# Optimization experiments

Measured on AMD Instinct MI355X. Metric: run time of the kernel, lower is better.

## Reference

```python
import jax, jax.numpy as jnp
import numpy as np

B, T, E, H, R = 1, 2048, 4096, 16, 64
D = E // H
SCALE_ATTN = float(np.sqrt(D))


def _i8_linear(x, W, b, alpha, beta):
    # W8A8B8O8Linear: int8 in, int8 weight/bias, int8 out with requant epilogue
    acc = jnp.einsum('bte,oe->bto', x.astype(jnp.int32), W.astype(jnp.int32)).astype(jnp.float32)
    y = alpha * acc + beta * b.astype(jnp.float32)
    return jnp.clip(jnp.round(y), -128, 127).astype(jnp.int8)


def _rotate_every_two(x):
    x1, x2 = x[..., ::2], x[..., 1::2]
    return jnp.stack([-x2, x1], axis=-1).reshape(x.shape)


def _sincos(seq_len, dim):
    inv_freq = 1.0 / (10000.0 ** (jnp.arange(0, dim, 2, dtype=jnp.float32) / dim))
    ang = jnp.arange(seq_len, dtype=jnp.float32)[:, None] * inv_freq[None, :]
    return jnp.sin(ang), jnp.cos(ang)


def _apply_rotary(x, sin, cos):
    # duplicate_interleave -> repeat each freq twice along last dim
    sin = jnp.repeat(sin, 2, axis=-1)[None, :, None, :]
    cos = jnp.repeat(cos, 2, axis=-1)[None, :, None, :]
    return x * cos + _rotate_every_two(x) * sin


def setup_inputs():
    key = jax.random.key(0)
    ks = jax.random.split(key, 9)
    i8 = lambda k, s: jax.random.randint(k, s, -128, 128, dtype=jnp.int32).astype(jnp.int8)
    return {
        'hidden_states': i8(ks[0], (B, T, E)),
        'Wq': i8(ks[1], (E, E)), 'bq': i8(ks[2], (E,)),
        'Wk': i8(ks[3], (E, E)), 'bk': i8(ks[4], (E,)),
        'Wv': i8(ks[5], (E, E)), 'bv': i8(ks[6], (E,)),
        'Wo': i8(ks[7], (E, E)),
        'b_out': jax.random.normal(ks[8], (E,), dtype=jnp.float32),
        'alpha_q': 2e-4, 'beta_q': 1.0,
        'alpha_k': 2e-4, 'beta_k': 1.0,
        'alpha_v': 2e-4, 'beta_v': 1.0,
        'alpha_qk': 1e-3, 'alpha_pv': 1e-2, 'alpha_out': 2e-4,
    }


def reference(hidden_states, Wq, bq, Wk, bk, Wv, bv, Wo, b_out,
              alpha_q, beta_q, alpha_k, beta_k, alpha_v, beta_v,
              alpha_qk, alpha_pv, alpha_out):
    # int8 q/k/v projections -> [B, T, H, D]
    q = _i8_linear(hidden_states, Wq, bq, alpha_q, beta_q).reshape(B, T, H, D)
    k = _i8_linear(hidden_states, Wk, bk, alpha_k, beta_k).reshape(B, T, H, D)
    v = _i8_linear(hidden_states, Wv, bv, alpha_v, beta_v).reshape(B, T, H, D)
    v = v.transpose(0, 2, 1, 3)  # [B, H, T, D] int8

    # fused rotary on first R dims (float math on dequantized-per-tensor int8 codes)
    sin, cos = _sincos(T, R)
    qf, kf = q.astype(jnp.float32), k.astype(jnp.float32)
    qf = jnp.concatenate([_apply_rotary(qf[..., :R], sin, cos), qf[..., R:]], axis=-1)
    kf = jnp.concatenate([_apply_rotary(kf[..., :R], sin, cos), kf[..., R:]], axis=-1)
    # torch .to(int8) truncates toward zero
    to_i8 = lambda x: jnp.clip(jnp.trunc(x), -128, 127).astype(jnp.int8)
    q = to_i8(qf.transpose(0, 2, 1, 3))  # [B, H, T, D]
    k = to_i8(kf.transpose(0, 2, 1, 3))

    scores = alpha_qk * jnp.einsum('bhtd,bhsd->bhts', q.astype(jnp.int32), k.astype(jnp.int32)).astype(jnp.float32)
    causal = jnp.tril(jnp.ones((T, T), dtype=bool))
    scores = jnp.where(causal, scores, jnp.finfo(jnp.float32).min)
    probs = jax.nn.softmax(scores / SCALE_ATTN, axis=-1)
    probs = jnp.round(probs * 127.0).astype(jnp.int8)  # requant probs to int8

    acc = jnp.einsum('bhts,bhsd->bhtd', probs.astype(jnp.int32), v.astype(jnp.int32)).astype(jnp.float32)
    attn_out = jnp.clip(jnp.round(alpha_pv * acc), -128, 127).astype(jnp.int8)
    attn_out = attn_out.transpose(0, 2, 1, 3).reshape(B, T, E)  # merge heads

    # W8A8BFP32OFP32Linear
    out = alpha_out * jnp.einsum('bte,oe->bto', attn_out.astype(jnp.int32), Wo.astype(jnp.int32)).astype(jnp.float32) + b_out
    return out
```

## Files before the change

kernel.cpp:

```cpp
#include <hip/hip_runtime.h>
#include <cstdint>
#include <cmath>

#define T_ 2048
#define E_ 4096
#define H_ 16
#define D_ 256
#define NF 32

typedef int v4i  __attribute__((ext_vector_type(4)));

__device__ __forceinline__ int dot4(int a, int b, int c) {
#if __has_builtin(__builtin_amdgcn_sdot4)
  return __builtin_amdgcn_sdot4(a, b, c, false);
#else
  c += ((a << 24) >> 24) * ((b << 24) >> 24);
  c += ((a << 16) >> 24) * ((b << 16) >> 24);
  c += ((a <<  8) >> 24) * ((b <<  8) >> 24);
  c += (a >> 24) * (b >> 24);
  return c;
#endif
}

__device__ __forceinline__ int pack4i(int4 v) {
  return (v.x & 255) | ((v.y & 255) << 8) | ((v.z & 255) << 16) | (v.w << 24);
}

#define GLD_LDS16(g, l)                                                        \
  __builtin_amdgcn_global_load_lds(                                            \
      (const __attribute__((address_space(1))) void*)(g),                      \
      (__attribute__((address_space(3))) void*)(l), 16, 0, 0)

__global__ void sincos_kernel(float* __restrict__ sinT, float* __restrict__ cosT) {
  int idx = blockIdx.x * 256 + threadIdx.x;
  int t = idx >> 5, j = idx & 31;
  float invf = (float)exp(-(double)j * (log(10000.0) / 32.0));
  float ang = (float)t * invf;
  sinT[idx] = (float)sin((double)ang);
  cosT[idx] = (float)cos((double)ang);
}

__global__ __launch_bounds__(256) void repack_kernel(const int* __restrict__ src,
                                                     int8_t* __restrict__ dst) {
  size_t i = (size_t)blockIdx.x * 256 + threadIdx.x;
  const int4* s = (const int4*)src + i * 4;
  int4 a = s[0], b = s[1], c = s[2], d = s[3];
  int4 o;
  o.x = pack4i(a); o.y = pack4i(b); o.z = pack4i(c); o.w = pack4i(d);
  ((int4*)dst)[i] = o;
}

__global__ __launch_bounds__(256, 3) void qkv_gemm_mfma(
    const int8_t* __restrict__ x8,
    const int8_t* __restrict__ Wq8, const int* __restrict__ bq,
    const int8_t* __restrict__ Wk8, const int* __restrict__ bk,
    const int8_t* __restrict__ Wv8, const int* __restrict__ bv,
    const float* __restrict__ alpq, const float* __restrict__ betq,
    const float* __restrict__ alpk, const float* __restrict__ betk,
    const float* __restrict__ alpv, const float* __restrict__ betv,
    int8_t* __restrict__ Q8, int8_t* __restrict__ K8, int8_t* __restrict__ VT)
{
  const int mode = blockIdx.z;
  const int8_t* __restrict__ W = (mode == 0) ? Wq8 : (mode == 1 ? Wk8 : Wv8);
  const int* __restrict__ bs   = (mode == 0) ? bq  : (mode == 1 ? bk  : bv);
  const float alpha = (mode == 0) ? alpq[0] : (mode == 1 ? alpk[0] : alpv[0]);
  const float beta  = (mode == 0) ? betq[0] : (mode == 1 ? betk[0] : betv[0]);

  __shared__ int8_t As[3][8192];
  __shared__ int8_t Bs[3][8192];

  const int tid  = threadIdx.x;
  const int wave = tid >> 6, lane = tid & 63;
  const int wm = wave >> 1, wn = wave & 1;
  const int t0 = blockIdx.x * 128, o0 = blockIdx.y * 128;

  const int srow = lane >> 2;
  const int scol = ((lane & 3) ^ ((lane >> 3) & 3)) * 16;
  const int col  = lane & 15;
  const int quad = lane >> 4;

  v4i acc[4][4] = {};

  const int8_t* gA0 = x8 + (size_t)(t0 + wave * 32 + srow) * E_ + scol;
  const int8_t* gB0 = W  + (size_t)(o0 + wave * 32 + srow) * E_ + scol;

#define STAGE_QKV(bufi, kt) do {                                               \
    const int e0_ = (kt) * 64;                                                 \
    GLD_LDS16(gA0 + e0_,           As[bufi] + wave * 2048);                    \
    GLD_LDS16(gA0 + e0_ + 16 * E_, As[bufi] + wave * 2048 + 1024);             \
    GLD_LDS16(gB0 + e0_,           Bs[bufi] + wave * 2048);                    \
    GLD_LDS16(gB0 + e0_ + 16 * E_, Bs[bufi] + wave * 2048 + 1024);             \
  } while (0)

  int aoff[4], boff[4];
  #pragma unroll
  for (int i = 0; i < 4; ++i) {
    const int ra = wm * 64 + i * 16 + col;
    aoff[i] = ra * 64 + ((quad ^ ((ra >> 1) & 3)) * 16);
    const int rb = wn * 64 + i * 16 + col;
    boff[i] = rb * 64 + ((quad ^ ((rb >> 1) & 3)) * 16);
  }

  STAGE_QKV(0, 0);
  STAGE_QKV(1, 1);

  int cur = 0;
  for (int kt = 0; kt < 64; ++kt) {
    if (kt == 63) asm volatile("s_waitcnt vmcnt(0)" ::: "memory");
    else          asm volatile("s_waitcnt vmcnt(4)" ::: "memory");
    __builtin_amdgcn_s_barrier();
    if (kt < 62) {
      int nb = cur + 2; if (nb >= 3) nb -= 3;
      STAGE_QKV(nb, kt + 2);
    }
    v4i a[4], b[4];
    #pragma unroll
    for (int i = 0; i < 4; ++i)
      a[i] = *(const v4i*)(As[cur] + aoff[i]);
    #pragma unroll
    for (int j = 0; j < 4; ++j)
      b[j] = *(const v4i*)(Bs[cur] + boff[j]);
    __builtin_amdgcn_s_setprio(1);
    #pragma unroll
    for (int i = 0; i < 4; ++i)
      #pragma unroll
      for (int j = 0; j < 4; ++j)
        acc[i][j] = __builtin_amdgcn_mfma_i32_16x16x64_i8(a[i], b[j], acc[i][j], 0, 0, 0);
    __builtin_amdgcn_s_setprio(0);
    cur = (cur == 2) ? 0 : cur + 1;
  }
#undef STAGE_QKV

  int8_t* __restrict__ dst = (mode == 0) ? Q8 : (mode == 1 ? K8 : VT);
  #pragma unroll
  for (int j = 0; j < 4; ++j) {
    const int o  = o0 + wn * 64 + j * 16 + col;
    const int h  = o >> 8;
    const int dd = o & 255;
    const float bb = (float)bs[o];
    #pragma unroll
    for (int i = 0; i < 4; ++i) {
      const int tb = t0 + wm * 64 + i * 16 + quad * 4;
      int qb[4];
      #pragma unroll
      for (int r = 0; r < 4; ++r) {
        float v = __fadd_rn(__fmul_rn(alpha, (float)acc[i][j][r]),
                            __fmul_rn(beta, bb));
        v = rintf(v);
        v = fminf(fmaxf(v, -128.0f), 127.0f);
        qb[r] = (int)v;
      }
      if (mode == 2) {
        int packed = (qb[0] & 255) | ((qb[1] & 255) << 8) |
                     ((qb[2] & 255) << 16) | ((qb[3] & 255) << 24);
        *(int*)(dst + ((size_t)h * 256 + dd) * T_ + tb) = packed;
      } else {
        #pragma unroll
        for (int r = 0; r < 4; ++r)
          dst[((size_t)h * T_ + tb + r) * D_ + dd] = (int8_t)qb[r];
      }
    }
  }
}

__global__ __launch_bounds__(256) void rope_kernel(
    int8_t* __restrict__ Q8, int8_t* __restrict__ K8,
    const float* __restrict__ sinT, const float* __restrict__ cosT)
{
  int idx = blockIdx.x * 256 + threadIdx.x;
  int c = idx & 3;
  int t = (idx >> 2) & (T_ - 1);
  int h = (idx >> 13) & (H_ - 1);
  int m = idx >> 17;
  int8_t* base = (m == 0 ? Q8 : K8) + ((size_t)h * T_ + t) * D_ + c * 16;
  int4 v = *(int4*)base;
  int u[4] = {v.x, v.y, v.z, v.w};
  const int jb = c * 8;
  #pragma unroll
  for (int ui = 0; ui < 4; ++ui) {
    const int j = jb + ui * 2;
    const float s0 = sinT[t * NF + j],     c0 = cosT[t * NF + j];
    const float s1 = sinT[t * NF + j + 1], c1 = cosT[t * NF + j + 1];
    const int w = u[ui];
    float y0 = (float)((w << 24) >> 24);
    float y1 = (float)((w << 16) >> 24);
    float y2 = (float)((w <<  8) >> 24);
    float y3 = (float)(w >> 24);
    float r0 = __fadd_rn(__fmul_rn(y0, c0), __fmul_rn(-y1, s0));
    float r1 = __fadd_rn(__fmul_rn(y1, c0), __fmul_rn( y0, s0));
    float r2 = __fadd_rn(__fmul_rn(y2, c1), __fmul_rn(-y3, s1));
    float r3 = __fadd_rn(__fmul_rn(y3, c1), __fmul_rn( y2, s1));
    int q0 = (int)fminf(fmaxf(truncf(r0), -128.0f), 127.0f);
    int q1 = (int)fminf(fmaxf(truncf(r1), -128.0f), 127.0f);
    int q2 = (int)fminf(fmaxf(truncf(r2), -128.0f), 127.0f);
    int q3 = (int)fminf(fmaxf(truncf(r3), -128.0f), 127.0f);
    u[ui] = (q0 & 255) | ((q1 & 255) << 8) | ((q2 & 255) << 16) | ((q3 & 255) << 24);
  }
  int4 ov; ov.x = u[0]; ov.y = u[1]; ov.z = u[2]; ov.w = u[3];
  *(int4*)base = ov;
}

__global__ __launch_bounds__(256, 3) void out_gemm_mfma(
    const int8_t* __restrict__ xa, const int8_t* __restrict__ Wo8,
    const float* __restrict__ b_out, const float* __restrict__ p_aout,
    float* __restrict__ out)
{
  const float alpha = p_aout[0];
  __shared__ int8_t As[3][8192];
  __shared__ int8_t Bs[3][8192];

  const int tid  = threadIdx.x;
  const int wave = tid >> 6, lane = tid & 63;
  const int wm = wave >> 1, wn = wave & 1;
  const int t0 = blockIdx.x * 128, o0 = blockIdx.y * 128;
  const int srow = lane >> 2;
  const int scol = ((lane & 3) ^ ((lane >> 3) & 3)) * 16;
  const int col = lane & 15, quad = lane >> 4;

  v4i acc[4][4] = {};
  const int8_t* gA0 = xa  + (size_t)(t0 + wave * 32 + srow) * E_ + scol;
  const int8_t* gB0 = Wo8 + (size_t)(o0 + wave * 32 + srow) * E_ + scol;

#define STAGE_OUT(bufi, kt) do {                                               \
    const int e0_ = (kt) * 64;                                                 \
    GLD_LDS16(gA0 + e0_,           As[bufi] + wave * 2048);                    \
    GLD_LDS16(gA0 + e0_ + 16 * E_, As[bufi] + wave * 2048 + 1024);             \
    GLD_LDS16(gB0 + e0_,           Bs[bufi] + wave * 2048);                    \
    GLD_LDS16(gB0 + e0_ + 16 * E_, Bs[bufi] + wave * 2048 + 1024);             \
  } while (0)

  int aoff[4], boff[4];
  #pragma unroll
  for (int i = 0; i < 4; ++i) {
    const int ra = wm * 64 + i * 16 + col;
    aoff[i] = ra * 64 + ((quad ^ ((ra >> 1) & 3)) * 16);
    const int rb = wn * 64 + i * 16 + col;
    boff[i] = rb * 64 + ((quad ^ ((rb >> 1) & 3)) * 16);
  }

  STAGE_OUT(0, 0);
  STAGE_OUT(1, 1);

  int cur = 0;
  for (int kt = 0; kt < 64; ++kt) {
    if (kt == 63) asm volatile("s_waitcnt vmcnt(0)" ::: "memory");
    else          asm volatile("s_waitcnt vmcnt(4)" ::: "memory");
    __builtin_amdgcn_s_barrier();
    if (kt < 62) {
      int nb = cur + 2; if (nb >= 3) nb -= 3;
      STAGE_OUT(nb, kt + 2);
    }
    v4i a[4], b[4];
    #pragma unroll
    for (int i = 0; i < 4; ++i)
      a[i] = *(const v4i*)(As[cur] + aoff[i]);
    #pragma unroll
    for (int j = 0; j < 4; ++j)
      b[j] = *(const v4i*)(Bs[cur] + boff[j]);
    __builtin_amdgcn_s_setprio(1);
    #pragma unroll
    for (int i = 0; i < 4; ++i)
      #pragma unroll
      for (int j = 0; j < 4; ++j)
        acc[i][j] = __builtin_amdgcn_mfma_i32_16x16x64_i8(a[i], b[j], acc[i][j], 0, 0, 0);
    __builtin_amdgcn_s_setprio(0);
    cur = (cur == 2) ? 0 : cur + 1;
  }
#undef STAGE_OUT

  #pragma unroll
  for (int j = 0; j < 4; ++j) {
    const int o = o0 + wn * 64 + j * 16 + col;
    const float bb = b_out[o];
    #pragma unroll
    for (int i = 0; i < 4; ++i) {
      #pragma unroll
      for (int r = 0; r < 4; ++r) {
        const int t = t0 + wm * 64 + i * 16 + quad * 4 + r;
        out[(size_t)t * E_ + o] = __fadd_rn(__fmul_rn(alpha, (float)acc[i][j][r]), bb);
      }
    }
  }
}

__global__ __launch_bounds__(256) void attn_ms_chunk(
    const int8_t* __restrict__ Q8, const int8_t* __restrict__ K8,
    const float* __restrict__ p_aqk,
    float* __restrict__ mPart, float* __restrict__ sPart)
{
  const int ch = blockIdx.x;
  const int qi = blockIdx.y;
  const int h  = blockIdx.z;
  if ((ch << 2) > qi) return;

  __shared__ int8_t Qs[4 * 4096];
  __shared__ int8_t KVs[16384];
  __shared__ float  mred[64][2];
  __shared__ float  sred[64][2];

  const int t0  = qi * 64;
  const int tid = threadIdx.x;
  const int wave = tid >> 6, lane = tid & 63;
  const int wm = wave >> 1, wn = wave & 1;
  const int col = lane & 15, quad = lane >> 4;
  const int srow = lane >> 2, scol = (lane & 3) * 16;
  const float aqk = p_aqk[0] * 0.0625f;

  {
    const int8_t* g = Q8 + ((size_t)h * T_ + t0 + wave * 16 + srow) * D_ + scol;
    #pragma unroll
    for (int c = 0; c < 4; ++c)
      GLD_LDS16(g + c * 64, Qs + c * 4096 + wave * 1024);
  }

  const int it0 = ch * 4;
  const int it1 = (it0 + 3 < qi) ? (it0 + 3) : qi;

  float m[8], sm[8];
  #pragma unroll
  for (int u = 0; u < 8; ++u) { m[u] = -INFINITY; sm[u] = 0.0f; }

  for (int it = it0; it <= it1; ++it) {
    const int s0 = it * 64;
    __syncthreads();
    {
      const int8_t* g = K8 + ((size_t)h * T_ + s0 + wave * 16 + srow) * D_ + scol;
      #pragma unroll
      for (int c = 0; c < 4; ++c)
        GLD_LDS16(g + c * 64, KVs + c * 4096 + wave * 1024);
    }
    __syncthreads();
    v4i accS[2][2] = {};
    #pragma unroll
    for (int c = 0; c < 4; ++c) {
      v4i a[2], b[2];
      #pragma unroll
      for (int i = 0; i < 2; ++i)
        a[i] = *(const v4i*)(Qs + c * 4096 + (wm * 32 + i * 16 + col) * 64 + quad * 16);
      #pragma unroll
      for (int j = 0; j < 2; ++j)
        b[j] = *(const v4i*)(KVs + c * 4096 + (wn * 32 + j * 16 + col) * 64 + quad * 16);
      #pragma unroll
      for (int i = 0; i < 2; ++i)
        #pragma unroll
        for (int j = 0; j < 2; ++j)
          accS[i][j] = __builtin_amdgcn_mfma_i32_16x16x64_i8(a[i], b[j], accS[i][j], 0, 0, 0);
    }
    const bool diag = (s0 == t0);
    #pragma unroll
    for (int i = 0; i < 2; ++i) {
      #pragma unroll
      for (int r = 0; r < 4; ++r) {
        const int ri = i * 4 + r;
        const int qrow = t0 + wm * 32 + i * 16 + quad * 4 + r;
        #pragma unroll
        for (int j = 0; j < 2; ++j) {
          const int s = s0 + wn * 32 + j * 16 + col;
          if (!diag || s <= qrow) {
            float l = __fmul_rn(aqk, (float)accS[i][j][r]);
            if (l > m[ri]) { sm[ri] = sm[ri] * expf(m[ri] - l) + 1.0f; m[ri] = l; }
            else           { sm[ri] += expf(l - m[ri]); }
          }
        }
      }
    }
  }

  #pragma unroll
  for (int u = 0; u < 8; ++u) {
    #pragma unroll
    for (int off = 1; off < 16; off <<= 1) {
      float om = __shfl_xor(m[u], off);
      float os = __shfl_xor(sm[u], off);
      float mm = fmaxf(m[u], om);
      float e1 = (m[u] == mm) ? 1.0f : expf(m[u] - mm);
      float e2 = (om   == mm) ? 1.0f : expf(om - mm);
      sm[u] = sm[u] * e1 + os * e2;
      m[u] = mm;
    }
  }
  __syncthreads();
  if (col == 0) {
    #pragma unroll
    for (int u = 0; u < 8; ++u) {
      int row = wm * 32 + (u >> 2) * 16 + quad * 4 + (u & 3);
      mred[row][wn] = m[u];
      sred[row][wn] = sm[u];
    }
  }
  __syncthreads();
  if (col == 0 && wn == 0) {
    #pragma unroll
    for (int u = 0; u < 8; ++u) {
      int row = wm * 32 + (u >> 2) * 16 + quad * 4 + (u & 3);
      float m0 = mred[row][0], m1 = mred[row][1];
      float sa = sred[row][0], sb = sred[row][1];
      float mm = fmaxf(m0, m1);
      float e0 = (m0 == mm) ? 1.0f : expf(m0 - mm);
      float e1 = (m1 == mm) ? 1.0f : expf(m1 - mm);
      size_t base = (((size_t)h * 32 + qi) * 64 + row) * 8 + ch;
      mPart[base] = mm;
      sPart[base] = __fadd_rn(__fmul_rn(sa, e0), __fmul_rn(sb, e1));
    }
  }
}

__global__ __launch_bounds__(256) void attn_ms_combine(
    const float* __restrict__ mPart, const float* __restrict__ sPart,
    float* __restrict__ mFg, float* __restrict__ sFg)
{
  int idx = blockIdx.x * 256 + threadIdx.x;
  int t = idx & (T_ - 1), h = idx >> 11;
  int qi = t >> 6, row = t & 63;
  int nch = (qi >> 2) + 1;
  const float* mp = mPart + (((size_t)h * 32 + qi) * 64 + row) * 8;
  const float* sp = sPart + (((size_t)h * 32 + qi) * 64 + row) * 8;
  float m = mp[0], s = sp[0];
  for (int c = 1; c < nch; ++c) {
    float mc = mp[c], sc = sp[c];
    float mm = fmaxf(m, mc);
    float e1 = (m  == mm) ? 1.0f : expf(m - mm);
    float e2 = (mc == mm) ? 1.0f : expf(mc - mm);
    s = __fadd_rn(__fmul_rn(s, e1), __fmul_rn(sc, e2));
    m = mm;
  }
  mFg[idx] = m;
  sFg[idx] = s;
}

__global__ __launch_bounds__(256) void attn_pv_chunk(
    const int8_t* __restrict__ Q8, const int8_t* __restrict__ K8,
    const int8_t* __restrict__ VT,
    const float* __restrict__ p_aqk,
    const float* __restrict__ mFg, const float* __restrict__ sFg,
    int* __restrict__ P0, int* __restrict__ P1)
{
  const int cc = blockIdx.x;
  const int qi = 31 - blockIdx.y;
  const int h  = blockIdx.z;
  if (cc == 1 && qi < 16) return;

  __shared__ int8_t Qs[4 * 4096];
  __shared__ int8_t KVs[16384];
  __shared__ int8_t Ps[64][64];

  const int t0  = qi * 64;
  const int tid = threadIdx.x;
  const int wave = tid >> 6, lane = tid & 63;
  const int wm = wave >> 1, wn = wave & 1;
  const int col = lane & 15, quad = lane >> 4;
  const int srow = lane >> 2, scol = (lane & 3) * 16;
  const float aqk = p_aqk[0] * 0.0625f;

  {
    const int8_t* g = Q8 + ((size_t)h * T_ + t0 + wave * 16 + srow) * D_ + scol;
    #pragma unroll
    for (int c = 0; c < 4; ++c)
      GLD_LDS16(g + c * 64, Qs + c * 4096 + wave * 1024);
  }

  float mF[8], sF[8];
  #pragma unroll
  for (int u = 0; u < 8; ++u) {
    const int row = wm * 32 + (u >> 2) * 16 + quad * 4 + (u & 3);
    mF[u] = mFg[h * T_ + t0 + row];
    sF[u] = sFg[h * T_ + t0 + row];
  }

  const int it0 = cc * 16;
  const int it1 = (it0 + 15 < qi) ? (it0 + 15) : qi;

  v4i pv[2][8] = {};
  for (int it = it0; it <= it1; ++it) {
    const int s0 = it * 64;
    __syncthreads();
    {
      const int8_t* g = K8 + ((size_t)h * T_ + s0 + wave * 16 + srow) * D_ + scol;
      #pragma unroll
      for (int c = 0; c < 4; ++c)
        GLD_LDS16(g + c * 64, KVs + c * 4096 + wave * 1024);
    }
    __syncthreads();
    v4i accS[2][2] = {};
    #pragma unroll
    for (int c = 0; c < 4; ++c) {
      v4i a[2], b[2];
      #pragma unroll
      for (int i = 0; i < 2; ++i)
        a[i] = *(const v4i*)(Qs + c * 4096 + (wm * 32 + i * 16 + col) * 64 + quad * 16);
      #pragma unroll
      for (int j = 0; j < 2; ++j)
        b[j] = *(const v4i*)(KVs + c * 4096 + (wn * 32 + j * 16 + col) * 64 + quad * 16);
      #pragma unroll
      for (int i = 0; i < 2; ++i)
        #pragma unroll
        for (int j = 0; j < 2; ++j)
          accS[i][j] = __builtin_amdgcn_mfma_i32_16x16x64_i8(a[i], b[j], accS[i][j], 0, 0, 0);
    }
    __syncthreads();
    {
      #pragma unroll
      for (int c = 0; c < 4; ++c) {
        const int drow = (wave * 4 + c) * 16 + srow;
        GLD_LDS16(VT + ((size_t)h * 256 + drow) * T_ + s0 + scol,
                  KVs + (wave * 4 + c) * 1024);
      }
    }
    const bool diag = (s0 == t0);
    #pragma unroll
    for (int i = 0; i < 2; ++i) {
      #pragma unroll
      for (int r = 0; r < 4; ++r) {
        const int ri = i * 4 + r;
        const int qrow = t0 + wm * 32 + i * 16 + quad * 4 + r;
        #pragma unroll
        for (int j = 0; j < 2; ++j) {
          const int s = s0 + wn * 32 + j * 16 + col;
          int q = 0;
          if (!diag || s <= qrow) {
            float l = __fmul_rn(aqk, (float)accS[i][j][r]);
            float p = expf(l - mF[ri]) / sF[ri];
            q = (int)rintf(__fmul_rn(p, 127.0f));
          }
          Ps[wm * 32 + i * 16 + quad * 4 + r][wn * 32 + j * 16 + col] = (int8_t)q;
        }
      }
    }
    __syncthreads();
    v4i a2[2], b2[8];
    #pragma unroll
    for (int i = 0; i < 2; ++i)
      a2[i] = *(const v4i*)&Ps[wm * 32 + i * 16 + col][quad * 16];
    #pragma unroll
    for (int dt = 0; dt < 8; ++dt)
      b2[dt] = *(const v4i*)(KVs + (wn * 128 + dt * 16 + col) * 64 + quad * 16);
    #pragma unroll
    for (int i = 0; i < 2; ++i)
      #pragma unroll
      for (int dt = 0; dt < 8; ++dt)
        pv[i][dt] = __builtin_amdgcn_mfma_i32_16x16x64_i8(a2[i], b2[dt], pv[i][dt], 0, 0, 0);
  }

  int* __restrict__ dst = (cc == 0)
      ? P0 + (((size_t)h * 32 + qi) << 14)
      : P1 + (((size_t)h * 16 + (qi - 16)) << 14);
  #pragma unroll
  for (int i = 0; i < 2; ++i) {
    #pragma unroll
    for (int r = 0; r < 4; ++r) {
      const int trow = wm * 32 + i * 16 + quad * 4 + r;
      #pragma unroll
      for (int dt = 0; dt < 8; ++dt) {
        const int d = wn * 128 + dt * 16 + col;
        dst[trow * 256 + d] = pv[i][dt][r];
      }
    }
  }
}

__global__ __launch_bounds__(256) void attn_pv_combine(
    const int* __restrict__ P0, const int* __restrict__ P1,
    const float* __restrict__ p_apv, int8_t* __restrict__ attn8)
{
  const float apv = p_apv[0];
  int idx = blockIdx.x * 256 + threadIdx.x;
  int d4  = idx & 63;
  int row = (idx >> 6) & 63;
  int qi  = (idx >> 12) & 31;
  int h   = idx >> 17;
  size_t off = (((size_t)h * 32 + qi) << 14) + row * 256 + d4 * 4;
  int4 a = *(const int4*)(P0 + off);
  if (qi >= 16) {
    size_t off1 = (((size_t)h * 16 + (qi - 16)) << 14) + row * 256 + d4 * 4;
    int4 b1 = *(const int4*)(P1 + off1);
    a.x += b1.x; a.y += b1.y; a.z += b1.z; a.w += b1.w;
  }
  int q[4];
  int vv[4] = {a.x, a.y, a.z, a.w};
  #pragma unroll
  for (int r = 0; r < 4; ++r) {
    float y = rintf(__fmul_rn(apv, (float)vv[r]));
    y = fminf(fmaxf(y, -128.0f), 127.0f);
    q[r] = (int)y;
  }
  int packed = (q[0] & 255) | ((q[1] & 255) << 8) | ((q[2] & 255) << 16) | ((q[3] & 255) << 24);
  int t = qi * 64 + row;
  *(int*)(attn8 + (size_t)t * E_ + h * D_ + d4 * 4) = packed;
}

__global__ __launch_bounds__(256) void attn_mfma(
    const int8_t* __restrict__ Q8, const int8_t* __restrict__ K8,
    const int8_t* __restrict__ VT,
    const float* __restrict__ p_aqk, const float* __restrict__ p_apv,
    int8_t* __restrict__ attn8)
{
  __shared__ int8_t Qs[4 * 4096];
  __shared__ int8_t KVs[16384];
  __shared__ int8_t Ps[64][64];
  __shared__ float  mred[64][2];
  __shared__ float  sred[64][2];

  const int h   = blockIdx.y;
  const int t0  = blockIdx.x * 64;
  const int tid = threadIdx.x;
  const int wave = tid >> 6, lane = tid & 63;
  const int wm = wave >> 1, wn = wave & 1;
  const int col = lane & 15, quad = lane >> 4;
  const int srow = lane >> 2, scol = (lane & 3) * 16;
  const float aqk = p_aqk[0] * 0.0625f;
  const float apv = p_apv[0];

  {
    const int8_t* g = Q8 + ((size_t)h * T_ + t0 + wave * 16 + srow) * D_ + scol;
    #pragma unroll
    for (int c = 0; c < 4; ++c)
      GLD_LDS16(g + c * 64, Qs + c * 4096 + wave * 1024);
  }

  const int nt = t0 / 64 + 1;

  float m[8], sm[8];
  #pragma unroll
  for (int u = 0; u < 8; ++u) { m[u] = -INFINITY; sm[u] = 0.0f; }

  for (int it = 0; it < nt; ++it) {
    const int s0 = it * 64;
    __syncthreads();
    {
      const int8_t* g = K8 + ((size_t)h * T_ + s0 + wave * 16 + srow) * D_ + scol;
      #pragma unroll
      for (int c = 0; c < 4; ++c)
        GLD_LDS16(g + c * 64, KVs + c * 4096 + wave * 1024);
    }
    __syncthreads();
    v4i accS[2][2] = {};
    #pragma unroll
    for (int c = 0; c < 4; ++c) {
      v4i a[2], b[2];
      #pragma unroll
      for (int i = 0; i < 2; ++i)
        a[i] = *(const v4i*)(Qs + c * 4096 + (wm * 32 + i * 16 + col) * 64 + quad * 16);
      #pragma unroll
      for (int j = 0; j < 2; ++j)
        b[j] = *(const v4i*)(KVs + c * 4096 + (wn * 32 + j * 16 + col) * 64 + quad * 16);
      #pragma unroll
      for (int i = 0; i < 2; ++i)
        #pragma unroll
        for (int j = 0; j < 2; ++j)
          accS[i][j] = __builtin_amdgcn_mfma_i32_16x16x64_i8(a[i], b[j], accS[i][j], 0, 0, 0);
    }
    const bool diag = (s0 == t0);
    #pragma unroll
    for (int i = 0; i < 2; ++i) {
      #pragma unroll
      for (int r = 0; r < 4; ++r) {
        const int ri = i * 4 + r;
        const int qrow = t0 + wm * 32 + i * 16 + quad * 4 + r;
        #pragma unroll
        for (int j = 0; j < 2; ++j) {
          const int s = s0 + wn * 32 + j * 16 + col;
          if (!diag || s <= qrow) {
            float l = __fmul_rn(aqk, (float)accS[i][j][r]);
            if (l > m[ri]) { sm[ri] = sm[ri] * expf(m[ri] - l) + 1.0f; m[ri] = l; }
            else           { sm[ri] += expf(l - m[ri]); }
          }
        }
      }
    }
  }

  #pragma unroll
  for (int u = 0; u < 8; ++u) {
    #pragma unroll
    for (int off = 1; off < 16; off <<= 1) {
      float om = __shfl_xor(m[u], off);
      float os = __shfl_xor(sm[u], off);
      float mm = fmaxf(m[u], om);
      float e1 = (m[u] == mm) ? 1.0f : expf(m[u] - mm);
      float e2 = (om   == mm) ? 1.0f : expf(om - mm);
      sm[u] = sm[u] * e1 + os * e2;
      m[u] = mm;
    }
  }
  __syncthreads();
  if (col == 0) {
    #pragma unroll
    for (int u = 0; u < 8; ++u) {
      int row = wm * 32 + (u >> 2) * 16 + quad * 4 + (u & 3);
      mred[row][wn] = m[u];
      sred[row][wn] = sm[u];
    }
  }
  __syncthreads();
  float mF[8], sF[8];
  #pragma unroll
  for (int u = 0; u < 8; ++u) {
    int row = wm * 32 + (u >> 2) * 16 + quad * 4 + (u & 3);
    float m0 = mred[row][0], m1 = mred[row][1];
    float sa = sred[row][0], sb = sred[row][1];
    float mm = fmaxf(m0, m1);
    float e0 = (m0 == mm) ? 1.0f : expf(m0 - mm);
    float e1 = (m1 == mm) ? 1.0f : expf(m1 - mm);
    mF[u] = mm;
    sF[u] = __fadd_rn(__fmul_rn(sa, e0), __fmul_rn(sb, e1));
  }

  v4i pv[2][8] = {};
  for (int it = 0; it < nt; ++it) {
    const int s0 = it * 64;
    __syncthreads();
    {
      const int8_t* g = K8 + ((size_t)h * T_ + s0 + wave * 16 + srow) * D_ + scol;
      #pragma unroll
      for (int c = 0; c < 4; ++c)
        GLD_LDS16(g + c * 64, KVs + c * 4096 + wave * 1024);
    }
    __syncthreads();
    v4i accS[2][2] = {};
    #pragma unroll
    for (int c = 0; c < 4; ++c) {
      v4i a[2], b[2];
      #pragma unroll
      for (int i = 0; i < 2; ++i)
        a[i] = *(const v4i*)(Qs + c * 4096 + (wm * 32 + i * 16 + col) * 64 + quad * 16);
      #pragma unroll
      for (int j = 0; j < 2; ++j)
        b[j] = *(const v4i*)(KVs + c * 4096 + (wn * 32 + j * 16 + col) * 64 + quad * 16);
      #pragma unroll
      for (int i = 0; i < 2; ++i)
        #pragma unroll
        for (int j = 0; j < 2; ++j)
          accS[i][j] = __builtin_amdgcn_mfma_i32_16x16x64_i8(a[i], b[j], accS[i][j], 0, 0, 0);
    }
    __syncthreads();
    {
      #pragma unroll
      for (int c = 0; c < 4; ++c) {
        const int drow = (wave * 4 + c) * 16 + srow;
        GLD_LDS16(VT + ((size_t)h * 256 + drow) * T_ + s0 + scol,
                  KVs + (wave * 4 + c) * 1024);
      }
    }
    const bool diag = (s0 == t0);
    #pragma unroll
    for (int i = 0; i < 2; ++i) {
      #pragma unroll
      for (int r = 0; r < 4; ++r) {
        const int ri = i * 4 + r;
        const int qrow = t0 + wm * 32 + i * 16 + quad * 4 + r;
        #pragma unroll
        for (int j = 0; j < 2; ++j) {
          const int s = s0 + wn * 32 + j * 16 + col;
          int q = 0;
          if (!diag || s <= qrow) {
            float l = __fmul_rn(aqk, (float)accS[i][j][r]);
            float p = expf(l - mF[ri]) / sF[ri];
            q = (int)rintf(__fmul_rn(p, 127.0f));
          }
          Ps[wm * 32 + i * 16 + quad * 4 + r][wn * 32 + j * 16 + col] = (int8_t)q;
        }
      }
    }
    __syncthreads();
    v4i a2[2], b2[8];
    #pragma unroll
    for (int i = 0; i < 2; ++i)
      a2[i] = *(const v4i*)&Ps[wm * 32 + i * 16 + col][quad * 16];
    #pragma unroll
    for (int dt = 0; dt < 8; ++dt)
      b2[dt] = *(const v4i*)(KVs + (wn * 128 + dt * 16 + col) * 64 + quad * 16);
    #pragma unroll
    for (int i = 0; i < 2; ++i)
      #pragma unroll
      for (int dt = 0; dt < 8; ++dt)
        pv[i][dt] = __builtin_amdgcn_mfma_i32_16x16x64_i8(a2[i], b2[dt], pv[i][dt], 0, 0, 0);
  }

  #pragma unroll
  for (int i = 0; i < 2; ++i) {
    #pragma unroll
    for (int r = 0; r < 4; ++r) {
      const int t = t0 + wm * 32 + i * 16 + quad * 4 + r;
      #pragma unroll
      for (int dt = 0; dt < 8; ++dt) {
        const int d = wn * 128 + dt * 16 + col;
        float y = rintf(__fmul_rn(apv, (float)pv[i][dt][r]));
        y = fminf(fmaxf(y, -128.0f), 127.0f);
        attn8[(size_t)t * E_ + h * D_ + d] = (int8_t)(int)y;
      }
    }
  }
}

__global__ __launch_bounds__(256) void qkv_gemm_fb(
    const int* __restrict__ xp,
    const int* __restrict__ Wqp, const int* __restrict__ bq,
    const int* __restrict__ Wkp, const int* __restrict__ bk,
    const int* __restrict__ Wvp, const int* __restrict__ bv,
    const float* __restrict__ alpq, const float* __restrict__ betq,
    const float* __restrict__ alpk, const float* __restrict__ betk,
    const float* __restrict__ alpv, const float* __restrict__ betv,
    const float* __restrict__ sinT, const float* __restrict__ cosT,
    int8_t* __restrict__ Q8, int8_t* __restrict__ K8, int8_t* __restrict__ VT)
{
  const int mode = blockIdx.z;
  const int* __restrict__ Wp = (mode == 0) ? Wqp : (mode == 1 ? Wkp : Wvp);
  const int* __restrict__ bs = (mode == 0) ? bq  : (mode == 1 ? bk  : bv);
  const float alpha = (mode == 0) ? alpq[0] : (mode == 1 ? alpk[0] : alpv[0]);
  const float beta  = (mode == 0) ? betq[0] : (mode == 1 ? betk[0] : betv[0]);

  __shared__ int As[64 * 17];
  __shared__ int Bs[64 * 17];
  const int tid = threadIdx.x;
  const int tx = tid & 15, ty = tid >> 4;
  const int t0 = blockIdx.x * 64, o0 = blockIdx.y * 64;
  const int lrow = tid >> 2, lc = tid & 3;
  int acc[4][4] = {};

  for (int e0 = 0; e0 < E_; e0 += 64) {
    const int* xr = xp + (size_t)(t0 + lrow) * E_ + e0 + lc * 16;
    const int* wr = Wp + (size_t)(o0 + lrow) * E_ + e0 + lc * 16;
    int a4[4], b4[4];
    #pragma unroll
    for (int u = 0; u < 4; ++u) a4[u] = pack4i(((const int4*)xr)[u]);
    #pragma unroll
    for (int u = 0; u < 4; ++u) b4[u] = pack4i(((const int4*)wr)[u]);
    __syncthreads();
    int* ap = &As[lrow * 17 + lc * 4];
    ap[0] = a4[0]; ap[1] = a4[1]; ap[2] = a4[2]; ap[3] = a4[3];
    int* bp = &Bs[lrow * 17 + lc * 4];
    bp[0] = b4[0]; bp[1] = b4[1]; bp[2] = b4[2]; bp[3] = b4[3];
    __syncthreads();
    #pragma unroll
    for (int kk = 0; kk < 16; ++kk) {
      int a[4], b[4];
      #pragma unroll
      for (int i = 0; i < 4; ++i) a[i] = As[(ty * 4 + i) * 17 + kk];
      #pragma unroll
      for (int j = 0; j < 4; ++j) b[j] = Bs[(tx * 4 + j) * 17 + kk];
      #pragma unroll
      for (int i = 0; i < 4; ++i)
        #pragma unroll
        for (int j = 0; j < 4; ++j)
          acc[i][j] = dot4(a[i], b[j], acc[i][j]);
    }
  }

  const int ob = o0 + tx * 4;
  const int h  = ob >> 8;
  const int dd = ob & 255;
  #pragma unroll
  for (int i = 0; i < 4; ++i) {
    const int t = t0 + ty * 4 + i;
    float y[4];
    #pragma unroll
    for (int j = 0; j < 4; ++j) {
      float v = __fadd_rn(__fmul_rn(alpha, (float)acc[i][j]),
                          __fmul_rn(beta, (float)bs[ob + j]));
      v = rintf(v);
      y[j] = fminf(fmaxf(v, -128.0f), 127.0f);
    }
    int q0, q1, q2, q3;
    if (mode < 2 && dd < 64) {
      const int j0 = dd >> 1;
      const float s0 = sinT[t * NF + j0],     c0 = cosT[t * NF + j0];
      const float s1 = sinT[t * NF + j0 + 1], c1 = cosT[t * NF + j0 + 1];
      float r0 = __fadd_rn(__fmul_rn(y[0], c0), __fmul_rn(-y[1], s0));
      float r1 = __fadd_rn(__fmul_rn(y[1], c0), __fmul_rn( y[0], s0));
      float r2 = __fadd_rn(__fmul_rn(y[2], c1), __fmul_rn(-y[3], s1));
      float r3 = __fadd_rn(__fmul_rn(y[3], c1), __fmul_rn( y[2], s1));
      q0 = (int)fminf(fmaxf(truncf(r0), -128.0f), 127.0f);
      q1 = (int)fminf(fmaxf(truncf(r1), -128.0f), 127.0f);
      q2 = (int)fminf(fmaxf(truncf(r2), -128.0f), 127.0f);
      q3 = (int)fminf(fmaxf(truncf(r3), -128.0f), 127.0f);
    } else {
      q0 = (int)y[0]; q1 = (int)y[1]; q2 = (int)y[2]; q3 = (int)y[3];
    }
    if (mode == 2) {
      VT[((size_t)h * 256 + dd + 0) * T_ + t] = (int8_t)q0;
      VT[((size_t)h * 256 + dd + 1) * T_ + t] = (int8_t)q1;
      VT[((size_t)h * 256 + dd + 2) * T_ + t] = (int8_t)q2;
      VT[((size_t)h * 256 + dd + 3) * T_ + t] = (int8_t)q3;
    } else {
      int8_t* dst = (mode == 0) ? Q8 : K8;
      int packed = (q0 & 255) | ((q1 & 255) << 8) | ((q2 & 255) << 16) | ((q3 & 255) << 24);
      *(int*)(dst + ((size_t)h * T_ + t) * D_ + dd) = packed;
    }
  }
}

__global__ __launch_bounds__(256) void out_gemm_fb(
    const int8_t* __restrict__ xa, const int* __restrict__ Wop,
    const float* __restrict__ b_out, const float* __restrict__ p_aout,
    float* __restrict__ out)
{
  __shared__ int As[64 * 17];
  __shared__ int Bs[64 * 17];
  const float alpha = p_aout[0];
  const int tid = threadIdx.x;
  const int tx = tid & 15, ty = tid >> 4;
  const int t0 = blockIdx.x * 64, o0 = blockIdx.y * 64;
  const int lrow = tid >> 2, lc = tid & 3;
  int acc[4][4] = {};

  for (int e0 = 0; e0 < E_; e0 += 64) {
    int4 av4 = *(const int4*)(xa + (size_t)(t0 + lrow) * E_ + e0 + lc * 16);
    const int* wr = Wop + (size_t)(o0 + lrow) * E_ + e0 + lc * 16;
    int b4[4];
    #pragma unroll
    for (int u = 0; u < 4; ++u) b4[u] = pack4i(((const int4*)wr)[u]);
    __syncthreads();
    int* ap = &As[lrow * 17 + lc * 4];
    ap[0] = av4.x; ap[1] = av4.y; ap[2] = av4.z; ap[3] = av4.w;
    int* bp = &Bs[lrow * 17 + lc * 4];
    bp[0] = b4[0]; bp[1] = b4[1]; bp[2] = b4[2]; bp[3] = b4[3];
    __syncthreads();
    #pragma unroll
    for (int kk = 0; kk < 16; ++kk) {
      int a[4], b[4];
      #pragma unroll
      for (int i = 0; i < 4; ++i) a[i] = As[(ty * 4 + i) * 17 + kk];
      #pragma unroll
      for (int j = 0; j < 4; ++j) b[j] = Bs[(tx * 4 + j) * 17 + kk];
      #pragma unroll
      for (int i = 0; i < 4; ++i)
        #pragma unroll
        for (int j = 0; j < 4; ++j)
          acc[i][j] = dot4(a[i], b[j], acc[i][j]);
    }
  }
  #pragma unroll
  for (int i = 0; i < 4; ++i) {
    const int t = t0 + ty * 4 + i;
    const int ob = o0 + tx * 4;
    #pragma unroll
    for (int j = 0; j < 4; ++j) {
      out[(size_t)t * E_ + ob + j] =
          __fadd_rn(__fmul_rn(alpha, (float)acc[i][j]), b_out[ob + j]);
    }
  }
}

extern "C" void kernel_launch(void* const* d_in, const int* in_sizes, int n_in,
                              void* d_out, int out_size, void* d_ws, size_t ws_size,
                              hipStream_t stream) {
  const int* hs   = (const int*)d_in[0];
  const int* Wq   = (const int*)d_in[1];
  const int* bq   = (const int*)d_in[2];
  const int* Wk   = (const int*)d_in[3];
  const int* bk   = (const int*)d_in[4];
  const int* Wv   = (const int*)d_in[5];
  const int* bv   = (const int*)d_in[6];
  const int* Wo   = (const int*)d_in[7];
  const float* b_out = (const float*)d_in[8];
  const float* aq   = (const float*)d_in[9];
  const float* btq  = (const float*)d_in[10];
  const float* ak   = (const float*)d_in[11];
  const float* btk  = (const float*)d_in[12];
  const float* av   = (const float*)d_in[13];
  const float* btv  = (const float*)d_in[14];
  const float* aqk  = (const float*)d_in[15];
  const float* apv  = (const float*)d_in[16];
  const float* aout = (const float*)d_in[17];

  const size_t SEG = (size_t)H_ * T_ * D_;
  char* ws = (char*)d_ws;
  int8_t* Q8    = (int8_t*)ws;
  int8_t* K8    = Q8 + SEG;
  int8_t* VT    = K8 + SEG;
  int8_t* attn8 = VT + SEG;
  int8_t* x8    = attn8;
  float*  sinT  = (float*)(ws + 4 * SEG);
  float*  cosT  = sinT + T_ * NF;
  int8_t* Wq8   = (int8_t*)(cosT + T_ * NF);
  int8_t* Wk8   = Wq8 + (size_t)E_ * E_;
  int8_t* Wv8   = Wk8 + (size_t)E_ * E_;
  int8_t* Wo8   = Wv8 + (size_t)E_ * E_;
  const size_t NEED = 4 * SEG + 2 * (size_t)T_ * NF * 4 + 4 * (size_t)E_ * E_;
  const bool big = (ws_size >= NEED);

  sincos_kernel<<<(T_ * NF) / 256, 256, 0, stream>>>(sinT, cosT);

  if (big) {
    repack_kernel<<<(T_ * E_ / 16) / 256, 256, 0, stream>>>(hs, x8);
    repack_kernel<<<(E_ * E_ / 16) / 256, 256, 0, stream>>>(Wq, Wq8);
    repack_kernel<<<(E_ * E_ / 16) / 256, 256, 0, stream>>>(Wk, Wk8);
    repack_kernel<<<(E_ * E_ / 16) / 256, 256, 0, stream>>>(Wv, Wv8);
    repack_kernel<<<(E_ * E_ / 16) / 256, 256, 0, stream>>>(Wo, Wo8);
    qkv_gemm_mfma<<<dim3(T_ / 128, E_ / 128, 3), 256, 0, stream>>>(
        x8, Wq8, bq, Wk8, bk, Wv8, bv, aq, btq, ak, btk, av, btv, Q8, K8, VT);
    rope_kernel<<<(2 * H_ * T_ * 4) / 256, 256, 0, stream>>>(Q8, K8, sinT, cosT);

    int*   P1g   = (int*)Wq8;
    int*   P0g   = (int*)Wk8;
    float* mPart = (float*)attn8;
    float* sPart = mPart + (size_t)H_ * 32 * 64 * 8;
    float* mFg   = sPart + (size_t)H_ * 32 * 64 * 8;
    float* sFg   = mFg + (size_t)H_ * T_;

    attn_ms_chunk<<<dim3(8, 32, H_), 256, 0, stream>>>(Q8, K8, aqk, mPart, sPart);
    attn_ms_combine<<<(H_ * T_) / 256, 256, 0, stream>>>(mPart, sPart, mFg, sFg);
    attn_pv_chunk<<<dim3(2, 32, H_), 256, 0, stream>>>(
        Q8, K8, VT, aqk, mFg, sFg, P0g, P1g);
    attn_pv_combine<<<(H_ * 32 * 64 * 64) / 256, 256, 0, stream>>>(
        P0g, P1g, apv, attn8);

    out_gemm_mfma<<<dim3(T_ / 128, E_ / 128), 256, 0, stream>>>(
        attn8, Wo8, b_out, aout, (float*)d_out);
  } else {
    qkv_gemm_fb<<<dim3(T_ / 64, E_ / 64, 3), 256, 0, stream>>>(
        hs, Wq, bq, Wk, bk, Wv, bv, aq, btq, ak, btk, av, btv,
        sinT, cosT, Q8, K8, VT);
    attn_mfma<<<dim3(T_ / 64, H_), 256, 0, stream>>>(Q8, K8, VT, aqk, apv, attn8);
    out_gemm_fb<<<dim3(T_ / 64, E_ / 64), 256, 0, stream>>>(
        attn8, Wo, b_out, aout, (float*)d_out);
  }
}
```

Baseline: 700.8 us.

## Fuse QKV GEMMs into one kernel with RoPE epilogue and merged repacks

Merges the three separate Q/K/V projection GEMM launches into one kernel that loads each activation tile once and multiplies it against all three weight tiles, keeping three accumulator sets per thread. RoPE is applied in the GEMM epilogue through lane shuffles, which removes the separate rope pass over Q and K. The five repack launches become one multi-target launch, and the softmax stats combine kernel is folded into the PV kernel. In exchange, register pressure roughly triples (occupancy bound lowered to 2), LDS pipelining goes from triple to double buffering with an extra barrier per iteration, and the combine work is now repeated in every PV block.

```diff
diff --git a/kernel.cpp b/kernel.cpp
--- a/kernel.cpp
+++ b/kernel.cpp
@@ -40,8 +40,19 @@
   cosT[idx] = (float)cos((double)ang);
 }
 
-__global__ __launch_bounds__(256) void repack_kernel(const int* __restrict__ src,
-                                                     int8_t* __restrict__ dst) {
+__global__ __launch_bounds__(256) void repack5_kernel(
+    const int* __restrict__ sx, const int* __restrict__ s1,
+    const int* __restrict__ s2, const int* __restrict__ s3,
+    const int* __restrict__ s4,
+    int8_t* __restrict__ dx, int8_t* __restrict__ d1,
+    int8_t* __restrict__ d2, int8_t* __restrict__ d3,
+    int8_t* __restrict__ d4) {
+  const int w = blockIdx.y;
+  if (w == 0 && blockIdx.x >= (T_ * E_ / 16) / 256) return;
+  const int* __restrict__ src =
+      (w == 0) ? sx : (w == 1 ? s1 : (w == 2 ? s2 : (w == 3 ? s3 : s4)));
+  int8_t* __restrict__ dst =
+      (w == 0) ? dx : (w == 1 ? d1 : (w == 2 ? d2 : (w == 3 ? d3 : d4)));
   size_t i = (size_t)blockIdx.x * 256 + threadIdx.x;
   const int4* s = (const int4*)src + i * 4;
   int4 a = s[0], b = s[1], c = s[2], d = s[3];
@@ -50,7 +61,7 @@
   ((int4*)dst)[i] = o;
 }
 
-__global__ __launch_bounds__(256, 3) void qkv_gemm_mfma(
+__global__ __launch_bounds__(256, 2) void qkv_fused_mfma(
     const int8_t* __restrict__ x8,
     const int8_t* __restrict__ Wq8, const int* __restrict__ bq,
     const int8_t* __restrict__ Wk8, const int* __restrict__ bk,
@@ -58,16 +69,11 @@
     const float* __restrict__ alpq, const float* __restrict__ betq,
     const float* __restrict__ alpk, const float* __restrict__ betk,
     const float* __restrict__ alpv, const float* __restrict__ betv,
+    const float* __restrict__ sinT, const float* __restrict__ cosT,
     int8_t* __restrict__ Q8, int8_t* __restrict__ K8, int8_t* __restrict__ VT)
 {
-  const int mode = blockIdx.z;
-  const int8_t* __restrict__ W = (mode == 0) ? Wq8 : (mode == 1 ? Wk8 : Wv8);
-  const int* __restrict__ bs   = (mode == 0) ? bq  : (mode == 1 ? bk  : bv);
-  const float alpha = (mode == 0) ? alpq[0] : (mode == 1 ? alpk[0] : alpv[0]);
-  const float beta  = (mode == 0) ? betq[0] : (mode == 1 ? betk[0] : betv[0]);
-
-  __shared__ int8_t As[3][8192];
-  __shared__ int8_t Bs[3][8192];
+  __shared__ int8_t As[2][8192];
+  __shared__ int8_t Bs[2][3][8192];
 
   const int tid  = threadIdx.x;
   const int wave = tid >> 6, lane = tid & 63;
@@ -79,17 +85,23 @@
   const int col  = lane & 15;
   const int quad = lane >> 4;
 
-  v4i acc[4][4] = {};
-
-  const int8_t* gA0 = x8 + (size_t)(t0 + wave * 32 + srow) * E_ + scol;
-  const int8_t* gB0 = W  + (size_t)(o0 + wave * 32 + srow) * E_ + scol;
-
-#define STAGE_QKV(bufi, kt) do {                                               \
+  v4i accQ[4][4] = {}, accK[4][4] = {}, accV[4][4] = {};
+
+  const int8_t* gA0 = x8  + (size_t)(t0 + wave * 32 + srow) * E_ + scol;
+  const int8_t* gBq = Wq8 + (size_t)(o0 + wave * 32 + srow) * E_ + scol;
+  const int8_t* gBk = Wk8 + (size_t)(o0 + wave * 32 + srow) * E_ + scol;
+  const int8_t* gBv = Wv8 + (size_t)(o0 + wave * 32 + srow) * E_ + scol;
+
+#define STAGE_F(bufi, kt) do {                                                 \
     const int e0_ = (kt) * 64;                                                 \
     GLD_LDS16(gA0 + e0_,           As[bufi] + wave * 2048);                    \
     GLD_LDS16(gA0 + e0_ + 16 * E_, As[bufi] + wave * 2048 + 1024);             \
-    GLD_LDS16(gB0 + e0_,           Bs[bufi] + wave * 2048);                    \
-    GLD_LDS16(gB0 + e0_ + 16 * E_, Bs[bufi] + wave * 2048 + 1024);             \
+    GLD_LDS16(gBq + e0_,           Bs[bufi][0] + wave * 2048);                 \
+    GLD_LDS16(gBq + e0_ + 16 * E_, Bs[bufi][0] + wave * 2048 + 1024);          \
+    GLD_LDS16(gBk + e0_,           Bs[bufi][1] + wave * 2048);                 \
+    GLD_LDS16(gBk + e0_ + 16 * E_, Bs[bufi][1] + wave * 2048 + 1024);          \
+    GLD_LDS16(gBv + e0_,           Bs[bufi][2] + wave * 2048);                 \
+    GLD_LDS16(gBv + e0_ + 16 * E_, Bs[bufi][2] + wave * 2048 + 1024);          \
   } while (0)
 
   int aoff[4], boff[4];
@@ -101,103 +113,102 @@
     boff[i] = rb * 64 + ((quad ^ ((rb >> 1) & 3)) * 16);
   }
 
-  STAGE_QKV(0, 0);
-  STAGE_QKV(1, 1);
-
-  int cur = 0;
+  STAGE_F(0, 0);
+  STAGE_F(1, 1);
+
   for (int kt = 0; kt < 64; ++kt) {
+    const int cur = kt & 1;
     if (kt == 63) asm volatile("s_waitcnt vmcnt(0)" ::: "memory");
-    else          asm volatile("s_waitcnt vmcnt(4)" ::: "memory");
+    else          asm volatile("s_waitcnt vmcnt(8)" ::: "memory");
     __builtin_amdgcn_s_barrier();
-    if (kt < 62) {
-      int nb = cur + 2; if (nb >= 3) nb -= 3;
-      STAGE_QKV(nb, kt + 2);
-    }
-    v4i a[4], b[4];
+    v4i a[4];
     #pragma unroll
     for (int i = 0; i < 4; ++i)
       a[i] = *(const v4i*)(As[cur] + aoff[i]);
-    #pragma unroll
-    for (int j = 0; j < 4; ++j)
-      b[j] = *(const v4i*)(Bs[cur] + boff[j]);
     __builtin_amdgcn_s_setprio(1);
-    #pragma unroll
-    for (int i = 0; i < 4; ++i)
-      #pragma unroll
-      for (int j = 0; j < 4; ++j)
-        acc[i][j] = __builtin_amdgcn_mfma_i32_16x16x64_i8(a[i], b[j], acc[i][j], 0, 0, 0);
+    {
+      v4i b[4];
+      #pragma unroll
+      for (int j = 0; j < 4; ++j) b[j] = *(const v4i*)(Bs[cur][0] + boff[j]);
+      #pragma unroll
+      for (int i = 0; i < 4; ++i)
+        #pragma unroll
+        for (int j = 0; j < 4; ++j)
+          accQ[i][j] = __builtin_amdgcn_mfma_i32_16x16x64_i8(a[i], b[j], accQ[i][j], 0, 0, 0);
+      #pragma unroll
+      for (int j = 0; j < 4; ++j) b[j] = *(const v4i*)(Bs[cur][1] + boff[j]);
+      #pragma unroll
+      for (int i = 0; i < 4; ++i)
+        #pragma unroll
+        for (int j = 0; j < 4; ++j)
+          accK[i][j] = __builtin_amdgcn_mfma_i32_16x16x64_i8(a[i], b[j], accK[i][j], 0, 0, 0);
+      #pragma unroll
+      for (int j = 0; j < 4; ++j) b[j] = *(const v4i*)(Bs[cur][2] + boff[j]);
+      #pragma unroll
+      for (int i = 0; i < 4; ++i)
+        #pragma unroll
+        for (int j = 0; j < 4; ++j)
+          accV[i][j] = __builtin_amdgcn_mfma_i32_16x16x64_i8(a[i], b[j], accV[i][j], 0, 0, 0);
+    }
     __builtin_amdgcn_s_setprio(0);
-    cur = (cur == 2) ? 0 : cur + 1;
-  }
-#undef STAGE_QKV
-
-  int8_t* __restrict__ dst = (mode == 0) ? Q8 : (mode == 1 ? K8 : VT);
-  #pragma unroll
-  for (int j = 0; j < 4; ++j) {
-    const int o  = o0 + wn * 64 + j * 16 + col;
-    const int h  = o >> 8;
-    const int dd = o & 255;
-    const float bb = (float)bs[o];
-    #pragma unroll
-    for (int i = 0; i < 4; ++i) {
-      const int tb = t0 + wm * 64 + i * 16 + quad * 4;
-      int qb[4];
-      #pragma unroll
-      for (int r = 0; r < 4; ++r) {
-        float v = __fadd_rn(__fmul_rn(alpha, (float)acc[i][j][r]),
-                            __fmul_rn(beta, bb));
-        v = rintf(v);
-        v = fminf(fmaxf(v, -128.0f), 127.0f);
-        qb[r] = (int)v;
+    __builtin_amdgcn_s_barrier();
+    if (kt + 2 < 64) STAGE_F(cur, kt + 2);
+  }
+#undef STAGE_F
+
+  const bool ropeWave = ((o0 & 128) == 0) && (wn == 0);
+  #pragma unroll
+  for (int m = 0; m < 3; ++m) {
+    const int* __restrict__ bsp = (m == 0) ? bq : (m == 1 ? bk : bv);
+    const float alpha = (m == 0) ? alpq[0] : (m == 1 ? alpk[0] : alpv[0]);
+    const float beta  = (m == 0) ? betq[0] : (m == 1 ? betk[0] : betv[0]);
+    int8_t* __restrict__ dst = (m == 0) ? Q8 : (m == 1 ? K8 : VT);
+    #pragma unroll
+    for (int j = 0; j < 4; ++j) {
+      const int o  = o0 + wn * 64 + j * 16 + col;
+      const int h  = o >> 8;
+      const int dd = o & 255;
+      const float bb = (float)bsp[o];
+      const int jj = dd >> 1;
+      #pragma unroll
+      for (int i = 0; i < 4; ++i) {
+        const int tb = t0 + wm * 64 + i * 16 + quad * 4;
+        int qb[4];
+        #pragma unroll
+        for (int r = 0; r < 4; ++r) {
+          float v = __fadd_rn(__fmul_rn(alpha, (float)(m == 0 ? accQ[i][j][r]
+                                         : (m == 1 ? accK[i][j][r] : accV[i][j][r]))),
+                              __fmul_rn(beta, bb));
+          v = rintf(v);
+          v = fminf(fmaxf(v, -128.0f), 127.0f);
+          qb[r] = (int)v;
+        }
+        if (m < 2 && ropeWave) {
+          #pragma unroll
+          for (int r = 0; r < 4; ++r) {
+            float y  = (float)qb[r];
+            float yo = __shfl_xor(y, 1);
+            const int t = tb + r;
+            const float s = sinT[t * NF + jj];
+            const float c = cosT[t * NF + jj];
+            float rv = ((col & 1) == 0)
+                ? __fadd_rn(__fmul_rn(y, c), __fmul_rn(-yo, s))
+                : __fadd_rn(__fmul_rn(y, c), __fmul_rn(yo, s));
+            qb[r] = (int)fminf(fmaxf(truncf(rv), -128.0f), 127.0f);
+          }
+        }
+        if (m == 2) {
+          int packed = (qb[0] & 255) | ((qb[1] & 255) << 8) |
+                       ((qb[2] & 255) << 16) | ((qb[3] & 255) << 24);
+          *(int*)(dst + ((size_t)h * 256 + dd) * T_ + tb) = packed;
+        } else {
+          #pragma unroll
+          for (int r = 0; r < 4; ++r)
+            dst[((size_t)h * T_ + tb + r) * D_ + dd] = (int8_t)qb[r];
+        }
       }
-      if (mode == 2) {
-        int packed = (qb[0] & 255) | ((qb[1] & 255) << 8) |
-                     ((qb[2] & 255) << 16) | ((qb[3] & 255) << 24);
-        *(int*)(dst + ((size_t)h * 256 + dd) * T_ + tb) = packed;
-      } else {
-        #pragma unroll
-        for (int r = 0; r < 4; ++r)
-          dst[((size_t)h * T_ + tb + r) * D_ + dd] = (int8_t)qb[r];
-      }
-    }
-  }
-}
-
-__global__ __launch_bounds__(256) void rope_kernel(
-    int8_t* __restrict__ Q8, int8_t* __restrict__ K8,
-    const float* __restrict__ sinT, const float* __restrict__ cosT)
-{
-  int idx = blockIdx.x * 256 + threadIdx.x;
-  int c = idx & 3;
-  int t = (idx >> 2) & (T_ - 1);
-  int h = (idx >> 13) & (H_ - 1);
-  int m = idx >> 17;
-  int8_t* base = (m == 0 ? Q8 : K8) + ((size_t)h * T_ + t) * D_ + c * 16;
-  int4 v = *(int4*)base;
-  int u[4] = {v.x, v.y, v.z, v.w};
-  const int jb = c * 8;
-  #pragma unroll
-  for (int ui = 0; ui < 4; ++ui) {
-    const int j = jb + ui * 2;
-    const float s0 = sinT[t * NF + j],     c0 = cosT[t * NF + j];
-    const float s1 = sinT[t * NF + j + 1], c1 = cosT[t * NF + j + 1];
-    const int w = u[ui];
-    float y0 = (float)((w << 24) >> 24);
-    float y1 = (float)((w << 16) >> 24);
-    float y2 = (float)((w <<  8) >> 24);
-    float y3 = (float)(w >> 24);
-    float r0 = __fadd_rn(__fmul_rn(y0, c0), __fmul_rn(-y1, s0));
-    float r1 = __fadd_rn(__fmul_rn(y1, c0), __fmul_rn( y0, s0));
-    float r2 = __fadd_rn(__fmul_rn(y2, c1), __fmul_rn(-y3, s1));
-    float r3 = __fadd_rn(__fmul_rn(y3, c1), __fmul_rn( y2, s1));
-    int q0 = (int)fminf(fmaxf(truncf(r0), -128.0f), 127.0f);
-    int q1 = (int)fminf(fmaxf(truncf(r1), -128.0f), 127.0f);
-    int q2 = (int)fminf(fmaxf(truncf(r2), -128.0f), 127.0f);
-    int q3 = (int)fminf(fmaxf(truncf(r3), -128.0f), 127.0f);
-    u[ui] = (q0 & 255) | ((q1 & 255) << 8) | ((q2 & 255) << 16) | ((q3 & 255) << 24);
-  }
-  int4 ov; ov.x = u[0]; ov.y = u[1]; ov.z = u[2]; ov.w = u[3];
-  *(int4*)base = ov;
+    }
+  }
 }
 
 __global__ __launch_bounds__(256, 3) void out_gemm_mfma(
@@ -405,34 +416,11 @@
   }
 }
 
-__global__ __launch_bounds__(256) void attn_ms_combine(
-    const float* __restrict__ mPart, const float* __restrict__ sPart,
-    float* __restrict__ mFg, float* __restrict__ sFg)
-{
-  int idx = blockIdx.x * 256 + threadIdx.x;
-  int t = idx & (T_ - 1), h = idx >> 11;
-  int qi = t >> 6, row = t & 63;
-  int nch = (qi >> 2) + 1;
-  const float* mp = mPart + (((size_t)h * 32 + qi) * 64 + row) * 8;
-  const float* sp = sPart + (((size_t)h * 32 + qi) * 64 + row) * 8;
-  float m = mp[0], s = sp[0];
-  for (int c = 1; c < nch; ++c) {
-    float mc = mp[c], sc = sp[c];
-    float mm = fmaxf(m, mc);
-    float e1 = (m  == mm) ? 1.0f : expf(m - mm);
-    float e2 = (mc == mm) ? 1.0f : expf(mc - mm);
-    s = __fadd_rn(__fmul_rn(s, e1), __fmul_rn(sc, e2));
-    m = mm;
-  }
-  mFg[idx] = m;
-  sFg[idx] = s;
-}
-
 __global__ __launch_bounds__(256) void attn_pv_chunk(
     const int8_t* __restrict__ Q8, const int8_t* __restrict__ K8,
     const int8_t* __restrict__ VT,
     const float* __restrict__ p_aqk,
-    const float* __restrict__ mFg, const float* __restrict__ sFg,
+    const float* __restrict__ mPart, const float* __restrict__ sPart,
     int* __restrict__ P0, int* __restrict__ P1)
 {
   const int cc = blockIdx.x;
@@ -460,11 +448,23 @@
   }
 
   float mF[8], sF[8];
+  const int nch = (qi >> 2) + 1;
   #pragma unroll
   for (int u = 0; u < 8; ++u) {
     const int row = wm * 32 + (u >> 2) * 16 + quad * 4 + (u & 3);
-    mF[u] = mFg[h * T_ + t0 + row];
-    sF[u] = sFg[h * T_ + t0 + row];
+    const float* mp = mPart + (((size_t)h * 32 + qi) * 64 + row) * 8;
+    const float* sp = sPart + (((size_t)h * 32 + qi) * 64 + row) * 8;
+    float m = mp[0], s = sp[0];
+    for (int c = 1; c < nch; ++c) {
+      float mc = mp[c], sc = sp[c];
+      float mm = fmaxf(m, mc);
+      float e1 = (m  == mm) ? 1.0f : expf(m - mm);
+      float e2 = (mc == mm) ? 1.0f : expf(mc - mm);
+      s = __fadd_rn(__fmul_rn(s, e1), __fmul_rn(sc, e2));
+      m = mm;
+    }
+    mF[u] = m;
+    sF[u] = s;
   }
 
   const int it0 = cc * 16;
@@ -982,26 +982,20 @@
   sincos_kernel<<<(T_ * NF) / 256, 256, 0, stream>>>(sinT, cosT);
 
   if (big) {
-    repack_kernel<<<(T_ * E_ / 16) / 256, 256, 0, stream>>>(hs, x8);
-    repack_kernel<<<(E_ * E_ / 16) / 256, 256, 0, stream>>>(Wq, Wq8);
-    repack_kernel<<<(E_ * E_ / 16) / 256, 256, 0, stream>>>(Wk, Wk8);
-    repack_kernel<<<(E_ * E_ / 16) / 256, 256, 0, stream>>>(Wv, Wv8);
-    repack_kernel<<<(E_ * E_ / 16) / 256, 256, 0, stream>>>(Wo, Wo8);
-    qkv_gemm_mfma<<<dim3(T_ / 128, E_ / 128, 3), 256, 0, stream>>>(
-        x8, Wq8, bq, Wk8, bk, Wv8, bv, aq, btq, ak, btk, av, btv, Q8, K8, VT);
-    rope_kernel<<<(2 * H_ * T_ * 4) / 256, 256, 0, stream>>>(Q8, K8, sinT, cosT);
+    repack5_kernel<<<dim3((E_ * E_ / 16) / 256, 5), 256, 0, stream>>>(
+        hs, Wq, Wk, Wv, Wo, x8, Wq8, Wk8, Wv8, Wo8);
+    qkv_fused_mfma<<<dim3(T_ / 128, E_ / 128), 256, 0, stream>>>(
+        x8, Wq8, bq, Wk8, bk, Wv8, bv, aq, btq, ak, btk, av, btv,
+        sinT, cosT, Q8, K8, VT);
 
     int*   P1g   = (int*)Wq8;
     int*   P0g   = (int*)Wk8;
     float* mPart = (float*)attn8;
     float* sPart = mPart + (size_t)H_ * 32 * 64 * 8;
-    float* mFg   = sPart + (size_t)H_ * 32 * 64 * 8;
-    float* sFg   = mFg + (size_t)H_ * T_;
 
     attn_ms_chunk<<<dim3(8, 32, H_), 256, 0, stream>>>(Q8, K8, aqk, mPart, sPart);
-    attn_ms_combine<<<(H_ * T_) / 256, 256, 0, stream>>>(mPart, sPart, mFg, sFg);
     attn_pv_chunk<<<dim3(2, 32, H_), 256, 0, stream>>>(
-        Q8, K8, VT, aqk, mFg, sFg, P0g, P1g);
+        Q8, K8, VT, aqk, mPart, sPart, P0g, P1g);
     attn_pv_combine<<<(H_ * 32 * 64 * 64) / 256, 256, 0, stream>>>(
         P0g, P1g, apv, attn8);
 
```

Measured after the change: 704.6 us. About the same (+0.5%).
